# Performance work log

Measured on AMD Instinct MI355X. Metric: run time of the kernel, lower is better.

The kernel has to match this reference:

```python
import jax, jax.numpy as jnp
import numpy as np

B = 262144
NUM_PLAYERS = 450
EMBED = 8


def _lin(x, w, b):
    return x @ w + b


def setup_inputs() -> dict:
    key = jax.random.key(0)
    ks = jax.random.split(key, 32)
    # state: 73 continuous features + 5 player ids stored as floats
    cont = jax.random.normal(ks[0], (B, 73), dtype=jnp.float32)
    pids = jax.random.randint(ks[1], (B, 5), 0, NUM_PLAYERS).astype(jnp.float32)
    state = jnp.concatenate([cont, pids], axis=1)

    def w(k, shape, fan_in):
        return jax.random.normal(k, shape, dtype=jnp.float32) * (2.0 / fan_in) ** 0.5

    base_in = 13 + EMBED + 32      # ctx(21) + pooled defender phi(32) = 53
    pass_in = 32 + base_in         # tm_phi(32) + base(53) = 85? no: 32+53=85 -> wait
    pass_in = 32 + (13 + EMBED) + 32  # tm_phi + ctx + def_pooled = 32+21+32 = 85
    # Match torch: pass_input = 32 + ctx_dim + 32 where ctx_dim = 13+embed = 21 -> 85?
    # torch: ctx_dim = 13 + embed_dim = 21; base_input = ctx_dim + 32 = 53; pass_input = 32 + ctx_dim + 32 = 85.
    # BUT forward concatenates [tm_phi, ctx, def_pooled] = 32 + 21 + 32 = 85. Consistent.
    pass_in = 85
    return {
        "state": state,
        "emb": jax.random.normal(ks[2], (NUM_PLAYERS, EMBED), dtype=jnp.float32),
        "wd1": w(ks[3], (4, 32), 4),   "bd1": jnp.zeros((32,), jnp.float32),
        "wd2": w(ks[4], (32, 32), 32), "bd2": jnp.zeros((32,), jnp.float32),
        "wt1": w(ks[5], (10 + EMBED, 32), 18), "bt1": jnp.zeros((32,), jnp.float32),
        "wt2": w(ks[6], (32, 32), 32),         "bt2": jnp.zeros((32,), jnp.float32),
        "wv1": w(ks[7], (base_in, 64), base_in), "bv1": jnp.zeros((64,), jnp.float32),
        "wv2": w(ks[8], (64, 32), 64),           "bv2": jnp.zeros((32,), jnp.float32),
        "wv3": w(ks[9], (32, 1), 32),            "bv3": jnp.zeros((1,), jnp.float32),
        "ws1": w(ks[10], (base_in, 32), base_in), "bs1": jnp.zeros((32,), jnp.float32),
        "ws2": w(ks[11], (32, 1), 32),            "bs2": jnp.zeros((1,), jnp.float32),
        "wp1": w(ks[12], (pass_in, 64), pass_in), "bp1": jnp.zeros((64,), jnp.float32),
        "wp2": w(ks[13], (64, 16), 64),           "bp2": jnp.zeros((16,), jnp.float32),
        "wp3": w(ks[14], (16, 1), 16),            "bp3": jnp.zeros((1,), jnp.float32),
    }


def reference(state, emb, wd1, bd1, wd2, bd2, wt1, bt1, wt2, bt2,
              wv1, bv1, wv2, bv2, wv3, bv3, ws1, bs1, ws2, bs2,
              wp1, bp1, wp2, bp2, wp3, bp3):
    b = state.shape[0]
    context = state[:, :11]
    tm_open = state[:, 11:15]
    tm_fg = state[:, 15:19]
    tm_dist = state[:, 19:23]
    def_pos = state[:, 23:33].reshape(b, 5, 2)
    tm_pos = state[:, 33:41].reshape(b, 4, 2)
    bh_vel = state[:, 41:43]
    def_vel = state[:, 43:53].reshape(b, 5, 2)
    tm_vel = state[:, 53:61].reshape(b, 4, 2)
    tm_lane_min = state[:, 61:65]
    tm_corridor = state[:, 65:69]
    tm_pass_dist = state[:, 69:73]

    pids = jnp.clip(state[:, 73:78].astype(jnp.int32), 0, NUM_PLAYERS - 1)
    bh_embed = emb[pids[:, 0]]            # [b, E]
    tm_embeds = emb[pids[:, 1:5]]         # [b, 4, E]

    # batched defender phi over 5 entities: [b,5,4] -> [b,5,32]
    d_feat = jnp.concatenate([def_pos, def_vel], axis=-1)
    d_h = jax.nn.relu(jax.nn.relu(d_feat @ wd1 + bd1) @ wd2 + bd2)
    def_pooled = d_h.mean(axis=1)         # [b, 32]

    ctx = jnp.concatenate([context, bh_vel, bh_embed], axis=1)   # [b, 21]
    base = jnp.concatenate([ctx, def_pooled], axis=1)            # [b, 53]

    value = jax.nn.relu(jax.nn.relu(base @ wv1 + bv1) @ wv2 + bv2) @ wv3 + bv3  # [b,1]
    a_shoot = jax.nn.relu(base @ ws1 + bs1) @ ws2 + bs2                          # [b,1]

    # batched teammate phi over 4 entities: [b,4,18] -> [b,4,32]
    t_feat = jnp.concatenate([
        tm_pos, tm_vel,
        tm_open[:, :, None], tm_fg[:, :, None], tm_dist[:, :, None],
        tm_lane_min[:, :, None], tm_corridor[:, :, None], tm_pass_dist[:, :, None],
        tm_embeds,
    ], axis=-1)
    tm_phi = jax.nn.relu(jax.nn.relu(t_feat @ wt1 + bt1) @ wt2 + bt2)  # [b,4,32]

    base_b = jnp.broadcast_to(base[:, None, :], (b, 4, base.shape[1]))
    p_in = jnp.concatenate([tm_phi, base_b], axis=-1)                   # [b,4,85]
    a_pass = (jax.nn.relu(jax.nn.relu(p_in @ wp1 + bp1) @ wp2 + bp2) @ wp3 + bp3)[..., 0]  # [b,4]
    a_pass = a_pass - a_pass.mean(axis=1, keepdims=True)

    q_shoot = value + a_shoot          # [b,1]
    q_passes = value + a_pass          # [b,4]
    return jnp.concatenate([q_shoot, q_passes], axis=1)
```

## Files before the change

kernel.cpp:

```cpp
#include <hip/hip_runtime.h>
#include <hip/hip_bf16.h>

#define THREADS 512

typedef short bf16x8 __attribute__((ext_vector_type(8)));
typedef float f32x4 __attribute__((ext_vector_type(4)));

union FragU { unsigned u[4]; bf16x8 v; };

__device__ __forceinline__ int swz(int row, int col) { return col ^ ((row & 7) << 2); }

__device__ __forceinline__ void split8(const float* x, FragU& hi, FragU& lo) {
#pragma unroll
    for (int i = 0; i < 4; ++i) {
        float a = x[2 * i], b = x[2 * i + 1];
        __hip_bfloat162 h2 = __float22bfloat162_rn(make_float2(a, b));
        float ra = __bfloat162float(h2.x), rb = __bfloat162float(h2.y);
        __hip_bfloat162 l2 = __float22bfloat162_rn(make_float2(a - ra, b - rb));
        unsigned hu, lu;
        __builtin_memcpy(&hu, &h2, 4);
        __builtin_memcpy(&lu, &l2, 4);
        hi.u[i] = hu; lo.u[i] = lu;
    }
}

__device__ __forceinline__ f32x4 mm3(const FragU& ah, const FragU& al,
                                     const FragU& bh, const FragU& bl, f32x4 acc) {
    acc = __builtin_amdgcn_mfma_f32_16x16x32_bf16(al.v, bh.v, acc, 0, 0, 0);
    acc = __builtin_amdgcn_mfma_f32_16x16x32_bf16(ah.v, bl.v, acc, 0, 0, 0);
    acc = __builtin_amdgcn_mfma_f32_16x16x32_bf16(ah.v, bh.v, acc, 0, 0, 0);
    return acc;
}

__device__ __forceinline__ void load_pair(const uint4* __restrict__ ws, int pair, int lane,
                                          FragU& hi, FragU& lo) {
    uint4 a = ws[pair * 128 + lane];
    uint4 b = ws[pair * 128 + 64 + lane];
    hi.u[0] = a.x; hi.u[1] = a.y; hi.u[2] = a.z; hi.u[3] = a.w;
    lo.u[0] = b.x; lo.u[1] = b.y; lo.u[2] = b.z; lo.u[3] = b.w;
}

__device__ __forceinline__ void buildA(const float* buf, int stride, int cbase,
                                       int m, int kf, int lane, FragU& hi, FragU& lo) {
    const int row = m * 16 + (lane & 15);
    const int c0 = cbase + kf * 32 + ((lane >> 4) * 8);
    const float* p = buf + row * stride;
    float x[8];
    *reinterpret_cast<float4*>(&x[0]) = *reinterpret_cast<const float4*>(p + swz(row, c0));
    *reinterpret_cast<float4*>(&x[4]) = *reinterpret_cast<const float4*>(p + swz(row, c0 + 4));
    split8(x, hi, lo);
}

__device__ __forceinline__ void storeC(float* buf, int stride, int m, int nf, int lane, f32x4 c) {
    const int col = nf * 16 + (lane & 15);
    const int r0 = (lane >> 4) * 4 + m * 16;
    buf[(r0 + 0) * stride + swz(r0 + 0, col)] = c[0];
    buf[(r0 + 1) * stride + swz(r0 + 1, col)] = c[1];
    buf[(r0 + 2) * stride + swz(r0 + 2, col)] = c[2];
    buf[(r0 + 3) * stride + swz(r0 + 3, col)] = c[3];
}

#define PB_D2  0
#define PB_T1  2
#define PB_T2  4
#define PB_P1T 6
#define PB_P1B 10
#define PB_P2  18
#define PB_V1  20
#define PB_V2  28
#define PB_S1  32
#define WS_BYTES (36 * 2048)

__global__ __launch_bounds__(64)
void prep_weights(const float* __restrict__ wd2, const float* __restrict__ wt1,
                  const float* __restrict__ wt2, const float* __restrict__ wp1,
                  const float* __restrict__ wp2, const float* __restrict__ wv1,
                  const float* __restrict__ wv2, const float* __restrict__ ws1,
                  uint4* __restrict__ wsout) {
    const int pair = blockIdx.x;
    const int lane = threadIdx.x;
    const int base_[10]  = {0, 2, 4, 6, 10, 18, 20, 28, 32, 36};
    const int kreal_[9]  = {32, 18, 32, 32, 53, 64, 53, 64, 53};
    const int n_[9]      = {32, 32, 32, 64, 64, 16, 64, 32, 32};
    const int nfc_[9]    = {2, 2, 2, 4, 4, 1, 4, 2, 2};
    const int roff_[9]   = {0, 0, 0, 0, 32, 0, 0, 0, 0};
    int g = 0;
    while (g < 8 && pair >= base_[g + 1]) ++g;
    const int local = pair - base_[g];
    const int kf = local / nfc_[g];
    const int nfi = local % nfc_[g];
    const float* W = (g == 0) ? wd2 : (g == 1) ? wt1 : (g == 2) ? wt2 :
                     (g == 3 || g == 4) ? wp1 : (g == 5) ? wp2 :
                     (g == 6) ? wv1 : (g == 7) ? wv2 : ws1;
    const int N = n_[g];
    float x[8];
#pragma unroll
    for (int j = 0; j < 8; ++j) {
        const int k = kf * 32 + (lane >> 4) * 8 + j;
        const int n = nfi * 16 + (lane & 15);
        x[j] = (k < kreal_[g]) ? W[(roff_[g] + k) * N + n] : 0.0f;
    }
    FragU hi, lo;
    split8(x, hi, lo);
    wsout[pair * 128 + lane]      = make_uint4(hi.u[0], hi.u[1], hi.u[2], hi.u[3]);
    wsout[pair * 128 + 64 + lane] = make_uint4(lo.u[0], lo.u[1], lo.u[2], lo.u[3]);
}

#define SB 64
#define SS 32
#define WAVE_F 2048

__global__ __launch_bounds__(THREADS)
void dueling_mfma(const float* __restrict__ state, const float* __restrict__ emb,
                  const float* __restrict__ wd1, const float* __restrict__ bd1,
                  const float* __restrict__ bd2, const float* __restrict__ bt1,
                  const float* __restrict__ bt2, const float* __restrict__ bv1,
                  const float* __restrict__ bv2, const float* __restrict__ wv3,
                  const float* __restrict__ bv3, const float* __restrict__ bs1,
                  const float* __restrict__ ws2, const float* __restrict__ bs2,
                  const float* __restrict__ bp1, const float* __restrict__ bp2,
                  const float* __restrict__ wp3,
                  const uint4* __restrict__ ws, float* __restrict__ out, int nrows) {
    __shared__ float smem[8 * WAVE_F];
    const int lane = threadIdx.x & 63;
    const int wave = threadIdx.x >> 6;
    const int r    = lane & 31;
    const int sub  = lane >> 5;
    const int row  = blockIdx.x * 256 + wave * 32 + r;
    const float* __restrict__ s = state + (long long)row * 78;

    float* BASE = smem + wave * WAVE_F;
    float* BUFA = BASE;
    float* BUFB = BASE + 32 * SS;
    const int c16 = lane & 15;

#pragma unroll
    for (int i = 0; i < 8; ++i)
        *reinterpret_cast<float4*>(BASE + i * 256 + lane * 4) = make_float4(0.f, 0.f, 0.f, 0.f);

    if (lane < 32) {
        int pid0 = (int)s[73];
        pid0 = pid0 < 0 ? 0 : (pid0 > 449 ? 449 : pid0);
        const float4 e0 = *(const float4*)(emb + pid0 * 8);
        const float4 e1 = *(const float4*)(emb + pid0 * 8 + 4);
        float* bp = BASE + r * SB;
        *reinterpret_cast<float4*>(bp + swz(r,  0)) = make_float4(s[0], s[1], s[2], s[3]);
        *reinterpret_cast<float4*>(bp + swz(r,  4)) = make_float4(s[4], s[5], s[6], s[7]);
        *reinterpret_cast<float4*>(bp + swz(r,  8)) = make_float4(s[8], s[9], s[10], s[41]);
        *reinterpret_cast<float4*>(bp + swz(r, 12)) = make_float4(s[42], e0.x, e0.y, e0.z);
        *reinterpret_cast<float4*>(bp + swz(r, 16)) = make_float4(e0.w, e1.x, e1.y, e1.z);
        bp[swz(r, 20)] = e1.w;
    }

    float pool[2][2][4];
#pragma unroll
    for (int m = 0; m < 2; ++m)
#pragma unroll
        for (int nf = 0; nf < 2; ++nf)
#pragma unroll
            for (int q = 0; q < 4; ++q) pool[m][nf][q] = 0.0f;

#pragma unroll 1
    for (int p = 0; p < 5; ++p) {
        const float f0 = s[23 + 2 * p], f1 = s[24 + 2 * p];
        const float f2 = s[43 + 2 * p], f3 = s[44 + 2 * p];
#pragma unroll
        for (int i2 = 0; i2 < 4; ++i2) {
            const int i = sub * 4 + i2;
            const float4 b4 = *(const float4*)(bd1 + i * 4);
            const float4 w0 = *(const float4*)(wd1 + 0 * 32 + i * 4);
            const float4 w1 = *(const float4*)(wd1 + 1 * 32 + i * 4);
            const float4 w2 = *(const float4*)(wd1 + 2 * 32 + i * 4);
            const float4 w3 = *(const float4*)(wd1 + 3 * 32 + i * 4);
            float4 hv;
            hv.x = fmaxf(fmaf(f0, w0.x, fmaf(f1, w1.x, fmaf(f2, w2.x, fmaf(f3, w3.x, b4.x)))), 0.f);
            hv.y = fmaxf(fmaf(f0, w0.y, fmaf(f1, w1.y, fmaf(f2, w2.y, fmaf(f3, w3.y, b4.y)))), 0.f);
            hv.z = fmaxf(fmaf(f0, w0.z, fmaf(f1, w1.z, fmaf(f2, w2.z, fmaf(f3, w3.z, b4.z)))), 0.f);
            hv.w = fmaxf(fmaf(f0, w0.w, fmaf(f1, w1.w, fmaf(f2, w2.w, fmaf(f3, w3.w, b4.w)))), 0.f);
            *reinterpret_cast<float4*>(BASE + r * SB + swz(r, 24 + i * 4)) = hv;
        }

        FragU ah[2], al[2];
#pragma unroll
        for (int m = 0; m < 2; ++m) buildA(BASE, SB, 24, m, 0, lane, ah[m], al[m]);
#pragma unroll
        for (int nf = 0; nf < 2; ++nf) {
            FragU bh, bl; load_pair(ws, PB_D2 + nf, lane, bh, bl);
            const float bias = bd2[nf * 16 + c16];
#pragma unroll
            for (int m = 0; m < 2; ++m) {
                f32x4 acc = {bias, bias, bias, bias};
                acc = mm3(ah[m], al[m], bh, bl, acc);
#pragma unroll
                for (int q = 0; q < 4; ++q) pool[m][nf][q] += fmaxf(acc[q], 0.0f);
            }
        }
    }
    BASE[r * SB + swz(r, 53)] = 0.0f;
    BASE[r * SB + swz(r, 54)] = 0.0f;
    BASE[r * SB + swz(r, 55)] = 0.0f;
#pragma unroll
    for (int m = 0; m < 2; ++m)
#pragma unroll
        for (int nf = 0; nf < 2; ++nf)
#pragma unroll
            for (int q = 0; q < 4; ++q) {
                const int rw = (lane >> 4) * 4 + q + m * 16;
                BASE[rw * SB + swz(rw, 21 + nf * 16 + c16)] = pool[m][nf][q] * 0.2f;
            }

    FragU Xh[2][2], Xl[2][2];
#pragma unroll
    for (int m = 0; m < 2; ++m)
#pragma unroll
        for (int kf = 0; kf < 2; ++kf)
            buildA(BASE, SB, 0, m, kf, lane, Xh[m][kf], Xl[m][kf]);

    float v2acc[2][2][4];
#pragma unroll
    for (int m = 0; m < 2; ++m)
#pragma unroll
        for (int nf = 0; nf < 2; ++nf) {
            const float b = bv2[nf * 16 + c16];
#pragma unroll
            for (int q = 0; q < 4; ++q) v2acc[m][nf][q] = b;
        }
#pragma unroll 1
    for (int half = 0; half < 2; ++half) {
#pragma unroll
        for (int nfl = 0; nfl < 2; ++nfl) {
            const int ng = half * 2 + nfl;
            FragU b0h, b0l, b1h, b1l;
            load_pair(ws, PB_V1 + ng, lane, b0h, b0l);
            load_pair(ws, PB_V1 + 4 + ng, lane, b1h, b1l);
            const float bias = bv1[ng * 16 + c16];
#pragma unroll
            for (int m = 0; m < 2; ++m) {
                f32x4 acc = {bias, bias, bias, bias};
                acc = mm3(Xh[m][0], Xl[m][0], b0h, b0l, acc);
                acc = mm3(Xh[m][1], Xl[m][1], b1h, b1l, acc);
#pragma unroll
                for (int q = 0; q < 4; ++q) acc[q] = fmaxf(acc[q], 0.0f);
                storeC(BUFA, SS, m, nfl, lane, acc);
            }
        }
        FragU ah[2], al[2];
#pragma unroll
        for (int m = 0; m < 2; ++m) buildA(BUFA, SS, 0, m, 0, lane, ah[m], al[m]);
#pragma unroll
        for (int nf = 0; nf < 2; ++nf) {
            FragU bh, bl; load_pair(ws, PB_V2 + half * 2 + nf, lane, bh, bl);
#pragma unroll
            for (int m = 0; m < 2; ++m) {
                f32x4 acc = {v2acc[m][nf][0], v2acc[m][nf][1], v2acc[m][nf][2], v2acc[m][nf][3]};
                acc = mm3(ah[m], al[m], bh, bl, acc);
#pragma unroll
                for (int q = 0; q < 4; ++q) v2acc[m][nf][q] = acc[q];
            }
        }
    }
#pragma unroll
    for (int m = 0; m < 2; ++m)
#pragma unroll
        for (int nf = 0; nf < 2; ++nf) {
            f32x4 rr = {fmaxf(v2acc[m][nf][0], 0.f), fmaxf(v2acc[m][nf][1], 0.f),
                        fmaxf(v2acc[m][nf][2], 0.f), fmaxf(v2acc[m][nf][3], 0.f)};
            storeC(BUFA, SS, m, nf, lane, rr);
        }
    float value = bv3[0];
#pragma unroll
    for (int c4 = 0; c4 < 8; ++c4) {
        float4 v = *reinterpret_cast<const float4*>(BUFA + r * SS + swz(r, c4 * 4));
        value = fmaf(v.x, wv3[c4 * 4], value);
        value = fmaf(v.y, wv3[c4 * 4 + 1], value);
        value = fmaf(v.z, wv3[c4 * 4 + 2], value);
        value = fmaf(v.w, wv3[c4 * 4 + 3], value);
    }

#pragma unroll
    for (int nf = 0; nf < 2; ++nf) {
        FragU b0h, b0l, b1h, b1l;
        load_pair(ws, PB_S1 + nf, lane, b0h, b0l);
        load_pair(ws, PB_S1 + 2 + nf, lane, b1h, b1l);
        const float bias = bs1[nf * 16 + c16];
#pragma unroll
        for (int m = 0; m < 2; ++m) {
            f32x4 acc = {bias, bias, bias, bias};
            acc = mm3(Xh[m][0], Xl[m][0], b0h, b0l, acc);
            acc = mm3(Xh[m][1], Xl[m][1], b1h, b1l, acc);
#pragma unroll
            for (int q = 0; q < 4; ++q) acc[q] = fmaxf(acc[q], 0.0f);
            storeC(BUFA, SS, m, nf, lane, acc);
        }
    }
    float ashoot = bs2[0];
#pragma unroll
    for (int c4 = 0; c4 < 8; ++c4) {
        float4 v = *reinterpret_cast<const float4*>(BUFA + r * SS + swz(r, c4 * 4));
        ashoot = fmaf(v.x, ws2[c4 * 4], ashoot);
        ashoot = fmaf(v.y, ws2[c4 * 4 + 1], ashoot);
        ashoot = fmaf(v.z, ws2[c4 * 4 + 2], ashoot);
        ashoot = fmaf(v.w, ws2[c4 * 4 + 3], ashoot);
    }

    float ap0 = 0.f, ap1 = 0.f, ap2 = 0.f, ap3 = 0.f;
#pragma unroll 1
    for (int j = 0; j < 4; ++j) {
        if (lane < 32) {
            int pid = (int)s[74 + j];
            pid = pid < 0 ? 0 : (pid > 449 ? 449 : pid);
            const float4 e0 = *(const float4*)(emb + pid * 8);
            const float4 e1 = *(const float4*)(emb + pid * 8 + 4);
            float* tp = BUFA + r * SS;
            *reinterpret_cast<float4*>(tp + swz(r,  0)) =
                make_float4(s[33 + 2 * j], s[34 + 2 * j], s[53 + 2 * j], s[54 + 2 * j]);
            *reinterpret_cast<float4*>(tp + swz(r,  4)) =
                make_float4(s[11 + j], s[15 + j], s[19 + j], s[61 + j]);
            *reinterpret_cast<float4*>(tp + swz(r,  8)) = make_float4(s[65 + j], s[69 + j], e0.x, e0.y);
            *reinterpret_cast<float4*>(tp + swz(r, 12)) = make_float4(e0.z, e0.w, e1.x, e1.y);
            *reinterpret_cast<float4*>(tp + swz(r, 16)) = make_float4(e1.z, e1.w, 0.f, 0.f);
            *reinterpret_cast<float4*>(tp + swz(r, 20)) = make_float4(0.f, 0.f, 0.f, 0.f);
            *reinterpret_cast<float4*>(tp + swz(r, 24)) = make_float4(0.f, 0.f, 0.f, 0.f);
            *reinterpret_cast<float4*>(tp + swz(r, 28)) = make_float4(0.f, 0.f, 0.f, 0.f);
        }
        {
            FragU ah[2], al[2];
#pragma unroll
            for (int m = 0; m < 2; ++m) buildA(BUFA, SS, 0, m, 0, lane, ah[m], al[m]);
#pragma unroll
            for (int nf = 0; nf < 2; ++nf) {
                FragU bh, bl; load_pair(ws, PB_T1 + nf, lane, bh, bl);
                const float bias = bt1[nf * 16 + c16];
#pragma unroll
                for (int m = 0; m < 2; ++m) {
                    f32x4 acc = {bias, bias, bias, bias};
                    acc = mm3(ah[m], al[m], bh, bl, acc);
#pragma unroll
                    for (int q = 0; q < 4; ++q) acc[q] = fmaxf(acc[q], 0.0f);
                    storeC(BUFB, SS, m, nf, lane, acc);
                }
            }
        }
        {
            FragU ah[2], al[2];
#pragma unroll
            for (int m = 0; m < 2; ++m) buildA(BUFB, SS, 0, m, 0, lane, ah[m], al[m]);
#pragma unroll
            for (int nf = 0; nf < 2; ++nf) {
                FragU bh, bl; load_pair(ws, PB_T2 + nf, lane, bh, bl);
                const float bias = bt2[nf * 16 + c16];
#pragma unroll
                for (int m = 0; m < 2; ++m) {
                    f32x4 acc = {bias, bias, bias, bias};
                    acc = mm3(ah[m], al[m], bh, bl, acc);
#pragma unroll
                    for (int q = 0; q < 4; ++q) acc[q] = fmaxf(acc[q], 0.0f);
                    storeC(BUFA, SS, m, nf, lane, acc);
                }
            }
        }
        FragU th[2], tl2[2];
#pragma unroll
        for (int m = 0; m < 2; ++m) buildA(BUFA, SS, 0, m, 0, lane, th[m], tl2[m]);

        float p2acc[2][4];
        {
            const float bq = bp2[c16];
#pragma unroll
            for (int m = 0; m < 2; ++m)
#pragma unroll
                for (int q = 0; q < 4; ++q) p2acc[m][q] = bq;
        }
#pragma unroll 1
        for (int half = 0; half < 2; ++half) {
#pragma unroll
            for (int nfl = 0; nfl < 2; ++nfl) {
                const int ng = half * 2 + nfl;
                FragU bth, btl, b0h, b0l, b1h, b1l;
                load_pair(ws, PB_P1T + ng, lane, bth, btl);
                load_pair(ws, PB_P1B + ng, lane, b0h, b0l);
                load_pair(ws, PB_P1B + 4 + ng, lane, b1h, b1l);
                const float bias = bp1[ng * 16 + c16];
#pragma unroll
                for (int m = 0; m < 2; ++m) {
                    f32x4 acc = {bias, bias, bias, bias};
                    acc = mm3(th[m], tl2[m], bth, btl, acc);
                    acc = mm3(Xh[m][0], Xl[m][0], b0h, b0l, acc);
                    acc = mm3(Xh[m][1], Xl[m][1], b1h, b1l, acc);
#pragma unroll
                    for (int q = 0; q < 4; ++q) acc[q] = fmaxf(acc[q], 0.0f);
                    storeC(BUFB, SS, m, nfl, lane, acc);
                }
            }
            FragU bh, bl; load_pair(ws, PB_P2 + half, lane, bh, bl);
#pragma unroll
            for (int m = 0; m < 2; ++m) {
                FragU ah, al; buildA(BUFB, SS, 0, m, 0, lane, ah, al);
                f32x4 acc = {p2acc[m][0], p2acc[m][1], p2acc[m][2], p2acc[m][3]};
                acc = mm3(ah, al, bh, bl, acc);
#pragma unroll
                for (int q = 0; q < 4; ++q) p2acc[m][q] = acc[q];
            }
        }
#pragma unroll
        for (int m = 0; m < 2; ++m) {
            f32x4 rr = {fmaxf(p2acc[m][0], 0.f), fmaxf(p2acc[m][1], 0.f),
                        fmaxf(p2acc[m][2], 0.f), fmaxf(p2acc[m][3], 0.f)};
            storeC(BUFB, SS, m, 0, lane, rr);
        }
        float ap = 0.0f;
#pragma unroll
        for (int c4 = 0; c4 < 4; ++c4) {
            float4 v = *reinterpret_cast<const float4*>(BUFB + r * SS + swz(r, c4 * 4));
            ap = fmaf(v.x, wp3[c4 * 4], ap);
            ap = fmaf(v.y, wp3[c4 * 4 + 1], ap);
            ap = fmaf(v.z, wp3[c4 * 4 + 2], ap);
            ap = fmaf(v.w, wp3[c4 * 4 + 3], ap);
        }
        if (j == 0) ap0 = ap;
        else if (j == 1) ap1 = ap;
        else if (j == 2) ap2 = ap;
        else ap3 = ap;
    }

    if (lane < 32) {
        const float am = 0.25f * (ap0 + ap1 + ap2 + ap3);
        float* __restrict__ o = out + (long long)row * 5;
        o[0] = value + ashoot;
        o[1] = value + ap0 - am;
        o[2] = value + ap1 - am;
        o[3] = value + ap2 - am;
        o[4] = value + ap3 - am;
    }
}

__global__ __launch_bounds__(256)
void dueling_fwd_valu(const float* __restrict__ state, const float* __restrict__ emb,
                      const float* __restrict__ wd1, const float* __restrict__ bd1,
                      const float* __restrict__ wd2, const float* __restrict__ bd2,
                      const float* __restrict__ wt1, const float* __restrict__ bt1,
                      const float* __restrict__ wt2, const float* __restrict__ bt2,
                      const float* __restrict__ wv1, const float* __restrict__ bv1,
                      const float* __restrict__ wv2, const float* __restrict__ bv2,
                      const float* __restrict__ wv3, const float* __restrict__ bv3,
                      const float* __restrict__ ws1, const float* __restrict__ bs1,
                      const float* __restrict__ ws2, const float* __restrict__ bs2,
                      const float* __restrict__ wp1, const float* __restrict__ bp1,
                      const float* __restrict__ wp2, const float* __restrict__ bp2,
                      const float* __restrict__ wp3, const float* __restrict__ bp3,
                      float* __restrict__ out, int nrows) {
    const int row = blockIdx.x * 256 + threadIdx.x;
    if (row >= nrows) return;
    const float* __restrict__ s = state + (long long)row * 78;
    float def_pooled[32];
#pragma unroll
    for (int n = 0; n < 32; ++n) def_pooled[n] = 0.0f;
#pragma unroll 1
    for (int p = 0; p < 5; ++p) {
        const float f0 = s[23 + 2 * p], f1 = s[24 + 2 * p], f2 = s[43 + 2 * p], f3 = s[44 + 2 * p];
        float h1[32];
#pragma unroll
        for (int n = 0; n < 32; ++n) {
            float a = bd1[n];
            a = fmaf(f0, wd1[n], a); a = fmaf(f1, wd1[32 + n], a);
            a = fmaf(f2, wd1[64 + n], a); a = fmaf(f3, wd1[96 + n], a);
            h1[n] = fmaxf(a, 0.0f);
        }
        float a2[32];
#pragma unroll
        for (int n = 0; n < 32; ++n) a2[n] = bd2[n];
#pragma unroll
        for (int k = 0; k < 32; ++k) {
            const float hk = h1[k];
#pragma unroll
            for (int n = 0; n < 32; ++n) a2[n] = fmaf(hk, wd2[k * 32 + n], a2[n]);
        }
#pragma unroll
        for (int n = 0; n < 32; ++n) def_pooled[n] += fmaxf(a2[n], 0.0f);
    }
    float base[53];
#pragma unroll
    for (int i = 0; i < 11; ++i) base[i] = s[i];
    base[11] = s[41]; base[12] = s[42];
    {
        int pid0 = (int)s[73];
        pid0 = pid0 < 0 ? 0 : (pid0 > 449 ? 449 : pid0);
        const float4 e0 = *(const float4*)(emb + pid0 * 8);
        const float4 e1 = *(const float4*)(emb + pid0 * 8 + 4);
        base[13] = e0.x; base[14] = e0.y; base[15] = e0.z; base[16] = e0.w;
        base[17] = e1.x; base[18] = e1.y; base[19] = e1.z; base[20] = e1.w;
    }
#pragma unroll
    for (int n = 0; n < 32; ++n) base[21 + n] = def_pooled[n] * 0.2f;
    float a_shoot;
    {
        float t[32];
#pragma unroll
        for (int n = 0; n < 32; ++n) t[n] = bs1[n];
#pragma unroll
        for (int k = 0; k < 53; ++k) {
            const float xk = base[k];
#pragma unroll
            for (int n = 0; n < 32; ++n) t[n] = fmaf(xk, ws1[k * 32 + n], t[n]);
        }
        a_shoot = bs2[0];
#pragma unroll
        for (int k = 0; k < 32; ++k) a_shoot = fmaf(fmaxf(t[k], 0.0f), ws2[k], a_shoot);
    }
    float value;
    {
        float h32[32];
#pragma unroll
        for (int n = 0; n < 32; ++n) h32[n] = bv2[n];
#pragma unroll
        for (int half = 0; half < 2; ++half) {
            float hh[32];
#pragma unroll
            for (int n = 0; n < 32; ++n) hh[n] = bv1[half * 32 + n];
#pragma unroll
            for (int k = 0; k < 53; ++k) {
                const float xk = base[k];
#pragma unroll
                for (int n = 0; n < 32; ++n) hh[n] = fmaf(xk, wv1[k * 64 + half * 32 + n], hh[n]);
            }
#pragma unroll
            for (int k = 0; k < 32; ++k) {
                const float xk = fmaxf(hh[k], 0.0f);
#pragma unroll
                for (int n = 0; n < 32; ++n) h32[n] = fmaf(xk, wv2[(half * 32 + k) * 32 + n], h32[n]);
            }
        }
        value = bv3[0];
#pragma unroll
        for (int k = 0; k < 32; ++k) value = fmaf(fmaxf(h32[k], 0.0f), wv3[k], value);
    }
    float pb[64];
#pragma unroll
    for (int n = 0; n < 64; ++n) pb[n] = bp1[n];
#pragma unroll
    for (int k = 0; k < 53; ++k) {
        const float xk = base[k];
#pragma unroll
        for (int n = 0; n < 64; ++n) pb[n] = fmaf(xk, wp1[(32 + k) * 64 + n], pb[n]);
    }
    float ap0 = 0.f, ap1 = 0.f, ap2 = 0.f, ap3 = 0.f;
#pragma unroll 1
    for (int j = 0; j < 4; ++j) {
        float t1[32];
        {
            float tf[18];
            tf[0] = s[33 + 2 * j]; tf[1] = s[34 + 2 * j];
            tf[2] = s[53 + 2 * j]; tf[3] = s[54 + 2 * j];
            tf[4] = s[11 + j]; tf[5] = s[15 + j]; tf[6] = s[19 + j];
            tf[7] = s[61 + j]; tf[8] = s[65 + j]; tf[9] = s[69 + j];
            int pid = (int)s[74 + j];
            pid = pid < 0 ? 0 : (pid > 449 ? 449 : pid);
            const float4 e0 = *(const float4*)(emb + pid * 8);
            const float4 e1 = *(const float4*)(emb + pid * 8 + 4);
            tf[10] = e0.x; tf[11] = e0.y; tf[12] = e0.z; tf[13] = e0.w;
            tf[14] = e1.x; tf[15] = e1.y; tf[16] = e1.z; tf[17] = e1.w;
#pragma unroll
            for (int n = 0; n < 32; ++n) t1[n] = bt1[n];
#pragma unroll
            for (int k = 0; k < 18; ++k) {
                const float xk = tf[k];
#pragma unroll
                for (int n = 0; n < 32; ++n) t1[n] = fmaf(xk, wt1[k * 32 + n], t1[n]);
            }
        }
        float t2[32];
#pragma unroll
        for (int n = 0; n < 32; ++n) t2[n] = bt2[n];
#pragma unroll
        for (int k = 0; k < 32; ++k) {
            const float xk = fmaxf(t1[k], 0.0f);
#pragma unroll
            for (int n = 0; n < 32; ++n) t2[n] = fmaf(xk, wt2[k * 32 + n], t2[n]);
        }
#pragma unroll
        for (int n = 0; n < 32; ++n) t2[n] = fmaxf(t2[n], 0.0f);
        float p2[16];
#pragma unroll
        for (int n = 0; n < 16; ++n) p2[n] = bp2[n];
#pragma unroll
        for (int half = 0; half < 2; ++half) {
            float phh[32];
#pragma unroll
            for (int n = 0; n < 32; ++n) phh[n] = pb[half * 32 + n];
#pragma unroll
            for (int k = 0; k < 32; ++k) {
                const float xk = t2[k];
#pragma unroll
                for (int n = 0; n < 32; ++n) phh[n] = fmaf(xk, wp1[k * 64 + half * 32 + n], phh[n]);
            }
#pragma unroll
            for (int k = 0; k < 32; ++k) {
                const float xk = fmaxf(phh[k], 0.0f);
#pragma unroll
                for (int n = 0; n < 16; ++n) p2[n] = fmaf(xk, wp2[(half * 32 + k) * 16 + n], p2[n]);
            }
        }
        float a = bp3[0];
#pragma unroll
        for (int k = 0; k < 16; ++k) a = fmaf(fmaxf(p2[k], 0.0f), wp3[k], a);
        if (j == 0) ap0 = a; else if (j == 1) ap1 = a; else if (j == 2) ap2 = a; else ap3 = a;
    }
    const float am = 0.25f * (ap0 + ap1 + ap2 + ap3);
    float* __restrict__ o = out + (long long)row * 5;
    o[0] = value + a_shoot;
    o[1] = value + ap0 - am;
    o[2] = value + ap1 - am;
    o[3] = value + ap2 - am;
    o[4] = value + ap3 - am;
}

extern "C" void kernel_launch(void* const* d_in, const int* in_sizes, int n_in,
                              void* d_out, int out_size, void* d_ws, size_t ws_size,
                              hipStream_t stream) {
    const float* state = (const float*)d_in[0];
    const float* emb   = (const float*)d_in[1];
    const float* wd1 = (const float*)d_in[2];  const float* bd1 = (const float*)d_in[3];
    const float* wd2 = (const float*)d_in[4];  const float* bd2 = (const float*)d_in[5];
    const float* wt1 = (const float*)d_in[6];  const float* bt1 = (const float*)d_in[7];
    const float* wt2 = (const float*)d_in[8];  const float* bt2 = (const float*)d_in[9];
    const float* wv1 = (const float*)d_in[10]; const float* bv1 = (const float*)d_in[11];
    const float* wv2 = (const float*)d_in[12]; const float* bv2 = (const float*)d_in[13];
    const float* wv3 = (const float*)d_in[14]; const float* bv3 = (const float*)d_in[15];
    const float* ws1 = (const float*)d_in[16]; const float* bs1 = (const float*)d_in[17];
    const float* ws2 = (const float*)d_in[18]; const float* bs2 = (const float*)d_in[19];
    const float* wp1 = (const float*)d_in[20]; const float* bp1 = (const float*)d_in[21];
    const float* wp2 = (const float*)d_in[22]; const float* bp2 = (const float*)d_in[23];
    const float* wp3 = (const float*)d_in[24]; const float* bp3 = (const float*)d_in[25];

    const int nrows = in_sizes[0] / 78;

    if (ws_size < (size_t)WS_BYTES || (nrows & 255) != 0) {
        const int blocks = (nrows + 255) / 256;
        dueling_fwd_valu<<<blocks, 256, 0, stream>>>(
            state, emb, wd1, bd1, wd2, bd2, wt1, bt1, wt2, bt2,
            wv1, bv1, wv2, bv2, wv3, bv3, ws1, bs1, ws2, bs2,
            wp1, bp1, wp2, bp2, wp3, bp3, (float*)d_out, nrows);
        return;
    }

    prep_weights<<<36, 64, 0, stream>>>(wd2, wt1, wt2, wp1, wp2, wv1, wv2, ws1,
                                        (uint4*)d_ws);
    dueling_mfma<<<nrows / 256, THREADS, 0, stream>>>(
        state, emb, wd1, bd1, bd2, bt1, bt2, bv1, bv2, wv3, bv3,
        bs1, ws2, bs2, bp1, bp2, wp3,
        (const uint4*)d_ws, (float*)d_out, nrows);
}
```

Baseline: 132.5 us.

## Store activations in LDS as pre-split bf16 hi/lo planes with padded strides

Intermediate activations are now split into bf16 high and low parts when written to shared memory, so building MFMA A-fragments becomes two 16-byte loads instead of float loads plus a split. The XOR swizzle is replaced by padded row strides (72/40 shorts, 36 floats for the dot-product buffers) to avoid bank conflicts. The split work moves to the store side, using per-element scalar conversions and 16-bit LDS stores. The layout of shared memory per wave changes to match.

```diff
diff --git a/kernel.cpp b/kernel.cpp
--- a/kernel.cpp
+++ b/kernel.cpp
@@ -5,10 +5,17 @@
 
 typedef short bf16x8 __attribute__((ext_vector_type(8)));
 typedef float f32x4 __attribute__((ext_vector_type(4)));
+typedef unsigned short u16;
 
 union FragU { unsigned u[4]; bf16x8 v; };
 
-__device__ __forceinline__ int swz(int row, int col) { return col ^ ((row & 7) << 2); }
+__device__ __forceinline__ void split1(float x, u16& h, u16& l) {
+    __hip_bfloat16 bh = __float2bfloat16(x);
+    float rh = __bfloat162float(bh);
+    __hip_bfloat16 bl = __float2bfloat16(x - rh);
+    __builtin_memcpy(&h, &bh, 2);
+    __builtin_memcpy(&l, &bl, 2);
+}
 
 __device__ __forceinline__ void split8(const float* x, FragU& hi, FragU& lo) {
 #pragma unroll
@@ -40,24 +47,28 @@
     lo.u[0] = b.x; lo.u[1] = b.y; lo.u[2] = b.z; lo.u[3] = b.w;
 }
 
-__device__ __forceinline__ void buildA(const float* buf, int stride, int cbase,
-                                       int m, int kf, int lane, FragU& hi, FragU& lo) {
-    const int row = m * 16 + (lane & 15);
-    const int c0 = cbase + kf * 32 + ((lane >> 4) * 8);
-    const float* p = buf + row * stride;
-    float x[8];
-    *reinterpret_cast<float4*>(&x[0]) = *reinterpret_cast<const float4*>(p + swz(row, c0));
-    *reinterpret_cast<float4*>(&x[4]) = *reinterpret_cast<const float4*>(p + swz(row, c0 + 4));
-    split8(x, hi, lo);
-}
-
-__device__ __forceinline__ void storeC(float* buf, int stride, int m, int nf, int lane, f32x4 c) {
+__device__ __forceinline__ void buildAp(const u16* bh, const u16* bl, int stride, int cbase,
+                                        int m, int kf, int lane, FragU& hi, FragU& lo) {
+    const int off = (m * 16 + (lane & 15)) * stride + cbase + kf * 32 + ((lane >> 4) * 8);
+    hi.v = *reinterpret_cast<const bf16x8*>(bh + off);
+    lo.v = *reinterpret_cast<const bf16x8*>(bl + off);
+}
+
+__device__ __forceinline__ void storeCp(u16* bh, u16* bl, int stride, int m, int nf, int lane,
+                                        f32x4 c) {
     const int col = nf * 16 + (lane & 15);
     const int r0 = (lane >> 4) * 4 + m * 16;
-    buf[(r0 + 0) * stride + swz(r0 + 0, col)] = c[0];
-    buf[(r0 + 1) * stride + swz(r0 + 1, col)] = c[1];
-    buf[(r0 + 2) * stride + swz(r0 + 2, col)] = c[2];
-    buf[(r0 + 3) * stride + swz(r0 + 3, col)] = c[3];
+#pragma unroll
+    for (int i = 0; i < 4; ++i) {
+        u16 h, l; split1(c[i], h, l);
+        bh[(r0 + i) * stride + col] = h;
+        bl[(r0 + i) * stride + col] = l;
+    }
+}
+
+__device__ __forceinline__ void storeCf(float* buf, int stride, int m, int nf, int lane, f32x4 c) {
+    float* p = buf + (((lane >> 4) * 4) + m * 16) * stride + nf * 16 + (lane & 15);
+    p[0] = c[0]; p[stride] = c[1]; p[2 * stride] = c[2]; p[3 * stride] = c[3];
 }
 
 #define PB_D2  0
@@ -106,9 +117,10 @@
     wsout[pair * 128 + 64 + lane] = make_uint4(lo.u[0], lo.u[1], lo.u[2], lo.u[3]);
 }
 
-#define SB 64
-#define SS 32
-#define WAVE_F 2048
+#define SBP 72
+#define SSP 40
+#define SDOT 36
+#define WAVE_USH 5120
 
 __global__ __launch_bounds__(THREADS)
 void dueling_mfma(const float* __restrict__ state, const float* __restrict__ emb,
@@ -121,7 +133,7 @@
                   const float* __restrict__ bp1, const float* __restrict__ bp2,
                   const float* __restrict__ wp3,
                   const uint4* __restrict__ ws, float* __restrict__ out, int nrows) {
-    __shared__ float smem[8 * WAVE_F];
+    __shared__ u16 smem[8 * WAVE_USH];
     const int lane = threadIdx.x & 63;
     const int wave = threadIdx.x >> 6;
     const int r    = lane & 31;
@@ -129,27 +141,40 @@
     const int row  = blockIdx.x * 256 + wave * 32 + r;
     const float* __restrict__ s = state + (long long)row * 78;
 
-    float* BASE = smem + wave * WAVE_F;
-    float* BUFA = BASE;
-    float* BUFB = BASE + 32 * SS;
+    u16* REG   = smem + wave * WAVE_USH;
+    u16* BASEh = REG;
+    u16* BASEl = REG + 2304;
+    u16* PAh   = REG;
+    u16* PAl   = REG + 1280;
+    u16* PBh   = REG + 2560;
+    u16* PBl   = REG + 3840;
+    float* DOTF = reinterpret_cast<float*>(REG + 2560);
     const int c16 = lane & 15;
 
-#pragma unroll
-    for (int i = 0; i < 8; ++i)
-        *reinterpret_cast<float4*>(BASE + i * 256 + lane * 4) = make_float4(0.f, 0.f, 0.f, 0.f);
+    {
+        uint4* z = reinterpret_cast<uint4*>(REG);
+#pragma unroll
+        for (int i = 0; i < 10; ++i) z[i * 64 + lane] = make_uint4(0u, 0u, 0u, 0u);
+    }
 
     if (lane < 32) {
         int pid0 = (int)s[73];
         pid0 = pid0 < 0 ? 0 : (pid0 > 449 ? 449 : pid0);
         const float4 e0 = *(const float4*)(emb + pid0 * 8);
         const float4 e1 = *(const float4*)(emb + pid0 * 8 + 4);
-        float* bp = BASE + r * SB;
-        *reinterpret_cast<float4*>(bp + swz(r,  0)) = make_float4(s[0], s[1], s[2], s[3]);
-        *reinterpret_cast<float4*>(bp + swz(r,  4)) = make_float4(s[4], s[5], s[6], s[7]);
-        *reinterpret_cast<float4*>(bp + swz(r,  8)) = make_float4(s[8], s[9], s[10], s[41]);
-        *reinterpret_cast<float4*>(bp + swz(r, 12)) = make_float4(s[42], e0.x, e0.y, e0.z);
-        *reinterpret_cast<float4*>(bp + swz(r, 16)) = make_float4(e0.w, e1.x, e1.y, e1.z);
-        bp[swz(r, 20)] = e1.w;
+        float f[21];
+#pragma unroll
+        for (int i = 0; i < 11; ++i) f[i] = s[i];
+        f[11] = s[41]; f[12] = s[42];
+        f[13] = e0.x; f[14] = e0.y; f[15] = e0.z; f[16] = e0.w;
+        f[17] = e1.x; f[18] = e1.y; f[19] = e1.z; f[20] = e1.w;
+        u16* bh = BASEh + r * SBP;
+        u16* bl = BASEl + r * SBP;
+#pragma unroll
+        for (int i = 0; i < 21; ++i) {
+            u16 h, l; split1(f[i], h, l);
+            bh[i] = h; bl[i] = l;
+        }
     }
 
     float pool[2][2][4];
@@ -172,17 +197,23 @@
             const float4 w1 = *(const float4*)(wd1 + 1 * 32 + i * 4);
             const float4 w2 = *(const float4*)(wd1 + 2 * 32 + i * 4);
             const float4 w3 = *(const float4*)(wd1 + 3 * 32 + i * 4);
-            float4 hv;
-            hv.x = fmaxf(fmaf(f0, w0.x, fmaf(f1, w1.x, fmaf(f2, w2.x, fmaf(f3, w3.x, b4.x)))), 0.f);
-            hv.y = fmaxf(fmaf(f0, w0.y, fmaf(f1, w1.y, fmaf(f2, w2.y, fmaf(f3, w3.y, b4.y)))), 0.f);
-            hv.z = fmaxf(fmaf(f0, w0.z, fmaf(f1, w1.z, fmaf(f2, w2.z, fmaf(f3, w3.z, b4.z)))), 0.f);
-            hv.w = fmaxf(fmaf(f0, w0.w, fmaf(f1, w1.w, fmaf(f2, w2.w, fmaf(f3, w3.w, b4.w)))), 0.f);
-            *reinterpret_cast<float4*>(BASE + r * SB + swz(r, 24 + i * 4)) = hv;
+            float hv[4];
+            hv[0] = fmaxf(fmaf(f0, w0.x, fmaf(f1, w1.x, fmaf(f2, w2.x, fmaf(f3, w3.x, b4.x)))), 0.f);
+            hv[1] = fmaxf(fmaf(f0, w0.y, fmaf(f1, w1.y, fmaf(f2, w2.y, fmaf(f3, w3.y, b4.y)))), 0.f);
+            hv[2] = fmaxf(fmaf(f0, w0.z, fmaf(f1, w1.z, fmaf(f2, w2.z, fmaf(f3, w3.z, b4.z)))), 0.f);
+            hv[3] = fmaxf(fmaf(f0, w0.w, fmaf(f1, w1.w, fmaf(f2, w2.w, fmaf(f3, w3.w, b4.w)))), 0.f);
+            u16* bh = BASEh + r * SBP + 24 + i * 4;
+            u16* bl = BASEl + r * SBP + 24 + i * 4;
+#pragma unroll
+            for (int e = 0; e < 4; ++e) {
+                u16 h, l; split1(hv[e], h, l);
+                bh[e] = h; bl[e] = l;
+            }
         }
 
         FragU ah[2], al[2];
 #pragma unroll
-        for (int m = 0; m < 2; ++m) buildA(BASE, SB, 24, m, 0, lane, ah[m], al[m]);
+        for (int m = 0; m < 2; ++m) buildAp(BASEh, BASEl, SBP, 24, m, 0, lane, ah[m], al[m]);
 #pragma unroll
         for (int nf = 0; nf < 2; ++nf) {
             FragU bh, bl; load_pair(ws, PB_D2 + nf, lane, bh, bl);
@@ -196,9 +227,9 @@
             }
         }
     }
-    BASE[r * SB + swz(r, 53)] = 0.0f;
-    BASE[r * SB + swz(r, 54)] = 0.0f;
-    BASE[r * SB + swz(r, 55)] = 0.0f;
+    BASEh[r * SBP + 53] = 0; BASEl[r * SBP + 53] = 0;
+    BASEh[r * SBP + 54] = 0; BASEl[r * SBP + 54] = 0;
+    BASEh[r * SBP + 55] = 0; BASEl[r * SBP + 55] = 0;
 #pragma unroll
     for (int m = 0; m < 2; ++m)
 #pragma unroll
@@ -206,7 +237,9 @@
 #pragma unroll
             for (int q = 0; q < 4; ++q) {
                 const int rw = (lane >> 4) * 4 + q + m * 16;
-                BASE[rw * SB + swz(rw, 21 + nf * 16 + c16)] = pool[m][nf][q] * 0.2f;
+                u16 h, l; split1(pool[m][nf][q] * 0.2f, h, l);
+                BASEh[rw * SBP + 21 + nf * 16 + c16] = h;
+                BASEl[rw * SBP + 21 + nf * 16 + c16] = l;
             }
 
     FragU Xh[2][2], Xl[2][2];
@@ -214,7 +247,7 @@
     for (int m = 0; m < 2; ++m)
 #pragma unroll
         for (int kf = 0; kf < 2; ++kf)
-            buildA(BASE, SB, 0, m, kf, lane, Xh[m][kf], Xl[m][kf]);
+            buildAp(BASEh, BASEl, SBP, 0, m, kf, lane, Xh[m][kf], Xl[m][kf]);
 
     float v2acc[2][2][4];
 #pragma unroll
@@ -241,12 +274,12 @@
                 acc = mm3(Xh[m][1], Xl[m][1], b1h, b1l, acc);
 #pragma unroll
                 for (int q = 0; q < 4; ++q) acc[q] = fmaxf(acc[q], 0.0f);
-                storeC(BUFA, SS, m, nfl, lane, acc);
+                storeCp(PAh, PAl, SSP, m, nfl, lane, acc);
             }
         }
         FragU ah[2], al[2];
 #pragma unroll
-        for (int m = 0; m < 2; ++m) buildA(BUFA, SS, 0, m, 0, lane, ah[m], al[m]);
+        for (int m = 0; m < 2; ++m) buildAp(PAh, PAl, SSP, 0, m, 0, lane, ah[m], al[m]);
 #pragma unroll
         for (int nf = 0; nf < 2; ++nf) {
             FragU bh, bl; load_pair(ws, PB_V2 + half * 2 + nf, lane, bh, bl);
@@ -265,12 +298,12 @@
         for (int nf = 0; nf < 2; ++nf) {
             f32x4 rr = {fmaxf(v2acc[m][nf][0], 0.f), fmaxf(v2acc[m][nf][1], 0.f),
                         fmaxf(v2acc[m][nf][2], 0.f), fmaxf(v2acc[m][nf][3], 0.f)};
-            storeC(BUFA, SS, m, nf, lane, rr);
+            storeCf(DOTF, SDOT, m, nf, lane, rr);
         }
     float value = bv3[0];
 #pragma unroll
     for (int c4 = 0; c4 < 8; ++c4) {
-        float4 v = *reinterpret_cast<const float4*>(BUFA + r * SS + swz(r, c4 * 4));
+        float4 v = *reinterpret_cast<const float4*>(DOTF + r * SDOT + c4 * 4);
         value = fmaf(v.x, wv3[c4 * 4], value);
         value = fmaf(v.y, wv3[c4 * 4 + 1], value);
         value = fmaf(v.z, wv3[c4 * 4 + 2], value);
@@ -290,13 +323,13 @@
             acc = mm3(Xh[m][1], Xl[m][1], b1h, b1l, acc);
 #pragma unroll
             for (int q = 0; q < 4; ++q) acc[q] = fmaxf(acc[q], 0.0f);
-            storeC(BUFA, SS, m, nf, lane, acc);
+            storeCf(DOTF, SDOT, m, nf, lane, acc);
         }
     }
     float ashoot = bs2[0];
 #pragma unroll
     for (int c4 = 0; c4 < 8; ++c4) {
-        float4 v = *reinterpret_cast<const float4*>(BUFA + r * SS + swz(r, c4 * 4));
+        float4 v = *reinterpret_cast<const float4*>(DOTF + r * SDOT + c4 * 4);
         ashoot = fmaf(v.x, ws2[c4 * 4], ashoot);
         ashoot = fmaf(v.y, ws2[c4 * 4 + 1], ashoot);
         ashoot = fmaf(v.z, ws2[c4 * 4 + 2], ashoot);
@@ -311,22 +344,27 @@
             pid = pid < 0 ? 0 : (pid > 449 ? 449 : pid);
             const float4 e0 = *(const float4*)(emb + pid * 8);
             const float4 e1 = *(const float4*)(emb + pid * 8 + 4);
-            float* tp = BUFA + r * SS;
-            *reinterpret_cast<float4*>(tp + swz(r,  0)) =
-                make_float4(s[33 + 2 * j], s[34 + 2 * j], s[53 + 2 * j], s[54 + 2 * j]);
-            *reinterpret_cast<float4*>(tp + swz(r,  4)) =
-                make_float4(s[11 + j], s[15 + j], s[19 + j], s[61 + j]);
-            *reinterpret_cast<float4*>(tp + swz(r,  8)) = make_float4(s[65 + j], s[69 + j], e0.x, e0.y);
-            *reinterpret_cast<float4*>(tp + swz(r, 12)) = make_float4(e0.z, e0.w, e1.x, e1.y);
-            *reinterpret_cast<float4*>(tp + swz(r, 16)) = make_float4(e1.z, e1.w, 0.f, 0.f);
-            *reinterpret_cast<float4*>(tp + swz(r, 20)) = make_float4(0.f, 0.f, 0.f, 0.f);
-            *reinterpret_cast<float4*>(tp + swz(r, 24)) = make_float4(0.f, 0.f, 0.f, 0.f);
-            *reinterpret_cast<float4*>(tp + swz(r, 28)) = make_float4(0.f, 0.f, 0.f, 0.f);
+            float tf[18];
+            tf[0] = s[33 + 2 * j]; tf[1] = s[34 + 2 * j];
+            tf[2] = s[53 + 2 * j]; tf[3] = s[54 + 2 * j];
+            tf[4] = s[11 + j]; tf[5] = s[15 + j]; tf[6] = s[19 + j];
+            tf[7] = s[61 + j]; tf[8] = s[65 + j]; tf[9] = s[69 + j];
+            tf[10] = e0.x; tf[11] = e0.y; tf[12] = e0.z; tf[13] = e0.w;
+            tf[14] = e1.x; tf[15] = e1.y; tf[16] = e1.z; tf[17] = e1.w;
+            u16* bh = PAh + r * SSP;
+            u16* bl = PAl + r * SSP;
+#pragma unroll
+            for (int i = 0; i < 18; ++i) {
+                u16 h, l; split1(tf[i], h, l);
+                bh[i] = h; bl[i] = l;
+            }
+#pragma unroll
+            for (int i = 18; i < 32; ++i) { bh[i] = 0; bl[i] = 0; }
         }
         {
             FragU ah[2], al[2];
 #pragma unroll
-            for (int m = 0; m < 2; ++m) buildA(BUFA, SS, 0, m, 0, lane, ah[m], al[m]);
+            for (int m = 0; m < 2; ++m) buildAp(PAh, PAl, SSP, 0, m, 0, lane, ah[m], al[m]);
 #pragma unroll
             for (int nf = 0; nf < 2; ++nf) {
                 FragU bh, bl; load_pair(ws, PB_T1 + nf, lane, bh, bl);
@@ -337,14 +375,14 @@
                     acc = mm3(ah[m], al[m], bh, bl, acc);
 #pragma unroll
                     for (int q = 0; q < 4; ++q) acc[q] = fmaxf(acc[q], 0.0f);
-                    storeC(BUFB, SS, m, nf, lane, acc);
+                    storeCp(PBh, PBl, SSP, m, nf, lane, acc);
                 }
             }
         }
         {
             FragU ah[2], al[2];
 #pragma unroll
-            for (int m = 0; m < 2; ++m) buildA(BUFB, SS, 0, m, 0, lane, ah[m], al[m]);
+            for (int m = 0; m < 2; ++m) buildAp(PBh, PBl, SSP, 0, m, 0, lane, ah[m], al[m]);
 #pragma unroll
             for (int nf = 0; nf < 2; ++nf) {
                 FragU bh, bl; load_pair(ws, PB_T2 + nf, lane, bh, bl);
@@ -355,13 +393,13 @@
                     acc = mm3(ah[m], al[m], bh, bl, acc);
 #pragma unroll
                     for (int q = 0; q < 4; ++q) acc[q] = fmaxf(acc[q], 0.0f);
-                    storeC(BUFA, SS, m, nf, lane, acc);
+                    storeCp(PAh, PAl, SSP, m, nf, lane, acc);
                 }
             }
         }
         FragU th[2], tl2[2];
 #pragma unroll
-        for (int m = 0; m < 2; ++m) buildA(BUFA, SS, 0, m, 0, lane, th[m], tl2[m]);
+        for (int m = 0; m < 2; ++m) buildAp(PAh, PAl, SSP, 0, m, 0, lane, th[m], tl2[m]);
 
         float p2acc[2][4];
         {
@@ -389,13 +427,13 @@
                     acc = mm3(Xh[m][1], Xl[m][1], b1h, b1l, acc);
 #pragma unroll
                     for (int q = 0; q < 4; ++q) acc[q] = fmaxf(acc[q], 0.0f);
-                    storeC(BUFB, SS, m, nfl, lane, acc);
+                    storeCp(PBh, PBl, SSP, m, nfl, lane, acc);
                 }
             }
             FragU bh, bl; load_pair(ws, PB_P2 + half, lane, bh, bl);
 #pragma unroll
             for (int m = 0; m < 2; ++m) {
-                FragU ah, al; buildA(BUFB, SS, 0, m, 0, lane, ah, al);
+                FragU ah, al; buildAp(PBh, PBl, SSP, 0, m, 0, lane, ah, al);
                 f32x4 acc = {p2acc[m][0], p2acc[m][1], p2acc[m][2], p2acc[m][3]};
                 acc = mm3(ah, al, bh, bl, acc);
 #pragma unroll
@@ -406,12 +444,12 @@
         for (int m = 0; m < 2; ++m) {
             f32x4 rr = {fmaxf(p2acc[m][0], 0.f), fmaxf(p2acc[m][1], 0.f),
                         fmaxf(p2acc[m][2], 0.f), fmaxf(p2acc[m][3], 0.f)};
-            storeC(BUFB, SS, m, 0, lane, rr);
+            storeCf(DOTF, SDOT, m, 0, lane, rr);
         }
         float ap = 0.0f;
 #pragma unroll
         for (int c4 = 0; c4 < 4; ++c4) {
-            float4 v = *reinterpret_cast<const float4*>(BUFB + r * SS + swz(r, c4 * 4));
+            float4 v = *reinterpret_cast<const float4*>(DOTF + r * SDOT + c4 * 4);
             ap = fmaf(v.x, wp3[c4 * 4], ap);
             ap = fmaf(v.y, wp3[c4 * 4 + 1], ap);
             ap = fmaf(v.z, wp3[c4 * 4 + 2], ap);
```

Result: slower. 144.0 us (+8.7%).
